# Optimization experiments

Hardware: AMD Instinct MI355X
Metric: run time of the kernel (lower is better)

Reference implementation:

```python
import jax, jax.numpy as jnp
import numpy as np

N_NODES = 100000
N_EDGES = 3200000
N_GRAPHS = 5000
N_LAYERS = 2
BN_EPS = 1e-5


def setup_inputs() -> dict:
    key = jax.random.key(0)
    ks = jax.random.split(key, 20)
    inp = {}
    inp['x'] = jax.random.normal(ks[0], (N_NODES, 14), dtype=jnp.float32)
    inp['edge_index'] = jax.random.randint(ks[1], (2, N_EDGES), 0, N_NODES, dtype=jnp.int64)
    inp['edge_attr'] = jax.random.uniform(ks[2], (N_EDGES, 3), dtype=jnp.float32)
    inp['batch'] = jnp.sort(jax.random.randint(ks[3], (N_NODES,), 0, N_GRAPHS, dtype=jnp.int64))
    s = 0.1
    inp['node_w'] = jax.random.normal(ks[4], (14, 32), dtype=jnp.float32) * s
    inp['node_b'] = jnp.zeros((32,), dtype=jnp.float32)
    inp['edge_w'] = jax.random.normal(ks[5], (3, 32), dtype=jnp.float32) * s
    inp['edge_b'] = jnp.zeros((32,), dtype=jnp.float32)
    inp['conv_w1'] = jax.random.normal(ks[6], (N_LAYERS, 32, 75), dtype=jnp.float32) * s
    inp['conv_b1'] = jnp.zeros((N_LAYERS, 75), dtype=jnp.float32)
    inp['conv_w2'] = jax.random.normal(ks[7], (N_LAYERS, 75, 32), dtype=jnp.float32) * s
    inp['conv_b2'] = jnp.zeros((N_LAYERS, 32), dtype=jnp.float32)
    inp['bn_g'] = jnp.ones((N_LAYERS, 32), dtype=jnp.float32)
    inp['bn_b'] = jnp.zeros((N_LAYERS, 32), dtype=jnp.float32)
    inp['lin1_w'] = jax.random.normal(ks[8], (32, 16), dtype=jnp.float32) * s
    inp['lin1_b'] = jnp.zeros((16,), dtype=jnp.float32)
    inp['lin2_w'] = jax.random.normal(ks[9], (16, 2), dtype=jnp.float32) * s
    inp['lin2_b'] = jnp.zeros((2,), dtype=jnp.float32)
    return inp


def _forward(x, edge_attr, node_w, node_b, edge_w, edge_b,
             conv_w1, conv_b1, conv_w2, conv_b2, bn_g, bn_b,
             lin1_w, lin1_b, lin2_w, lin2_b, edge_index, batch):
    src, dst = edge_index[0], edge_index[1]
    h = x @ node_w + node_b                      # [N, 32]
    ea = edge_attr @ edge_w + edge_b             # [E, 32]
    for l in range(N_LAYERS):
        # GINEConv (eps=0): nn(x_i + sum_j relu(x_j + e_ji))
        msg = jax.nn.relu(h[src] + ea)           # [E, 32]
        agg = jax.ops.segment_sum(msg, dst, num_segments=N_NODES)
        z = h + agg
        z = jax.nn.relu(z @ conv_w1[l] + conv_b1[l]) @ conv_w2[l] + conv_b2[l]
        # BatchNorm1d (training-mode batch statistics)
        mu = jnp.mean(z, axis=0)
        var = jnp.var(z, axis=0)
        z = (z - mu) * jax.lax.rsqrt(var + BN_EPS) * bn_g[l] + bn_b[l]
        h = jax.nn.relu(z)
    # global_mean_pool
    sums = jax.ops.segment_sum(h, batch, num_segments=N_GRAPHS)   # [G, 32]
    counts = jax.ops.segment_sum(jnp.ones((h.shape[0],), h.dtype), batch, num_segments=N_GRAPHS)
    graph_x = sums / jnp.maximum(counts, 1.0)[:, None]
    pred = jax.nn.relu(graph_x @ lin1_w + lin1_b) @ lin2_w + lin2_b  # [G, 2]
    return pred


def reference(x, edge_index, edge_attr, batch, node_w, node_b, edge_w, edge_b,
              conv_w1, conv_b1, conv_w2, conv_b2, bn_g, bn_b,
              lin1_w, lin1_b, lin2_w, lin2_b):
    return _forward(x, edge_attr, node_w, node_b, edge_w, edge_b,
                    conv_w1, conv_b1, conv_w2, conv_b2, bn_g, bn_b,
                    lin1_w, lin1_b, lin2_w, lin2_b, edge_index, batch)
```

## Files before the change

### kernel.cpp

```cpp
#include <hip/hip_runtime.h>
#include <hip/hip_fp16.h>

#define N_NODES 100000
#define N_EDGES 3200000
#define N_GRAPHS 5000
#define BN_EPS 1e-5f
#define HPAD 80
#define CHUNK 2048
#define NBLKA 1563
#define NBKT 392
#define NPAD2 (NBKT * 256)
#define NBLK_TOT (NBKT * NBLKA)
#define NS1 2394
#define LALLOC (NS1 * 256)
#define W1S 36

__global__ void k_encode(const float* __restrict__ x, const float* __restrict__ W,
                         const float* __restrict__ b, float* __restrict__ h,
                         __half* __restrict__ h16) {
    __shared__ float sW[448];
    __shared__ float sb[32];
    for (int i = threadIdx.x; i < 448; i += 256) sW[i] = W[i];
    if (threadIdx.x < 32) sb[threadIdx.x] = b[threadIdx.x];
    __syncthreads();
    int n = blockIdx.x * 256 + threadIdx.x;
    if (n >= N_NODES) return;
    float xi[14];
#pragma unroll
    for (int k = 0; k < 14; k++) xi[k] = x[n * 14 + k];
    float4* hp = (float4*)(h + (size_t)n * 32);
    __half2* hq = (__half2*)(h16 + (size_t)n * 32);
#pragma unroll
    for (int q = 0; q < 8; q++) {
        float4 acc;
        float* ap = (float*)&acc;
#pragma unroll
        for (int i = 0; i < 4; i++) {
            int c = q * 4 + i;
            float a = sb[c];
#pragma unroll
            for (int k = 0; k < 14; k++) a += xi[k] * sW[k * 32 + c];
            ap[i] = a;
        }
        hp[q] = acc;
        hq[q * 2 + 0] = __floats2half2_rn(acc.x, acc.y);
        hq[q * 2 + 1] = __floats2half2_rn(acc.z, acc.w);
    }
}

__global__ void k_prep(const float* __restrict__ W1, const float* __restrict__ b1,
                       const float* __restrict__ W2,
                       float* __restrict__ w1tp, float* __restrict__ b1p,
                       float* __restrict__ w2p) {
    int i = blockIdx.x * 256 + threadIdx.x;
    if (i < 2 * HPAD * 32) {
        int l = i / (HPAD * 32), r = i % (HPAD * 32);
        int j = r / 32, c = r % 32;
        w1tp[i] = (j < 75) ? W1[l * 2400 + c * 75 + j] : 0.f;
        w2p[i]  = (j < 75) ? W2[l * 2400 + j * 32 + c] : 0.f;
    } else if (i < 2 * HPAD * 32 + 2 * HPAD) {
        int k = i - 2 * HPAD * 32;
        int l = k / HPAD, j = k % HPAD;
        b1p[k] = (j < 75) ? b1[l * 75 + j] : 0.f;
    }
}

__global__ void __launch_bounds__(256) ksA(const int* __restrict__ ei, int* __restrict__ cmat) {
    __shared__ int lh[NBKT];
    for (int i = threadIdx.x; i < NBKT; i += 256) lh[i] = 0;
    __syncthreads();
    int b0 = blockIdx.x * CHUNK;
    for (int i = threadIdx.x; i < CHUNK; i += 256) {
        int e = b0 + i;
        if (e < N_EDGES) atomicAdd(&lh[ei[N_EDGES + e] >> 8], 1);
    }
    __syncthreads();
    for (int i = threadIdx.x; i < NBKT; i += 256)
        cmat[i * NBLKA + blockIdx.x] = lh[i];
}

__global__ void ks1(const int* __restrict__ a, int* __restrict__ bs) {
    __shared__ int s[256];
    int i = blockIdx.x * 256 + threadIdx.x;
    s[threadIdx.x] = a[i];
    __syncthreads();
    for (int o = 128; o > 0; o >>= 1) {
        if (threadIdx.x < o) s[threadIdx.x] += s[threadIdx.x + o];
        __syncthreads();
    }
    if (threadIdx.x == 0) bs[blockIdx.x] = s[0];
}

template<int NSX, int VPTX>
__global__ void ks2(int* __restrict__ bs) {
    __shared__ int s[256];
    int t = threadIdx.x;
    int v[VPTX];
    int base = t * VPTX, sum = 0;
#pragma unroll
    for (int k = 0; k < VPTX; k++) {
        int idx = base + k;
        int x = (idx < NSX) ? bs[idx] : 0;
        v[k] = sum; sum += x;
    }
    s[t] = sum;
    __syncthreads();
    for (int o = 1; o < 256; o <<= 1) {
        int add = (t >= o) ? s[t - o] : 0;
        __syncthreads();
        s[t] += add;
        __syncthreads();
    }
    int excl = (t == 0) ? 0 : s[t - 1];
#pragma unroll
    for (int k = 0; k < VPTX; k++) {
        int idx = base + k;
        if (idx < NSX) bs[idx] = excl + v[k];
    }
}

__global__ void ks3(int* __restrict__ a, const int* __restrict__ bs) {
    __shared__ int s[256];
    int t = threadIdx.x, i = blockIdx.x * 256 + t;
    int v = a[i];
    s[t] = v;
    __syncthreads();
    for (int o = 1; o < 256; o <<= 1) {
        int add = (t >= o) ? s[t - o] : 0;
        __syncthreads();
        s[t] += add;
        __syncthreads();
    }
    a[i] = s[t] - v + bs[blockIdx.x];
}

__global__ void __launch_bounds__(256) ksB(const int* __restrict__ ei, const float* __restrict__ ea,
                                           const int* __restrict__ cmat, float4* __restrict__ buf1,
                                           unsigned char* __restrict__ key) {
    __shared__ float4 rec[CHUNK];
    __shared__ unsigned short sbkt[CHUNK];
    __shared__ int lh[NBKT];
    __shared__ int lex[NBKT];
    __shared__ int gb[NBKT];
    __shared__ int sc[256];
    int t = threadIdx.x;
    int b0 = blockIdx.x * CHUNK;
    int nval = min(CHUNK, N_EDGES - b0);
    for (int i = t; i < NBKT; i += 256) lh[i] = 0;
    __syncthreads();
    for (int i = t; i < nval; i += 256)
        atomicAdd(&lh[ei[N_EDGES + b0 + i] >> 8], 1);
    __syncthreads();
    int x0 = (t * 2 < NBKT) ? lh[t * 2] : 0;
    int x1 = (t * 2 + 1 < NBKT) ? lh[t * 2 + 1] : 0;
    int v0 = 0, v1 = x0, run = x0 + x1;
    sc[t] = run;
    __syncthreads();
    for (int o = 1; o < 256; o <<= 1) {
        int add = (t >= o) ? sc[t - o] : 0;
        __syncthreads();
        sc[t] += add;
        __syncthreads();
    }
    int excl = (t == 0) ? 0 : sc[t - 1];
    if (t * 2 < NBKT) {
        int base = excl + v0;
        lex[t * 2] = base; lh[t * 2] = base;
        gb[t * 2] = cmat[(t * 2) * NBLKA + blockIdx.x];
    }
    if (t * 2 + 1 < NBKT) {
        int base = excl + v1;
        lex[t * 2 + 1] = base; lh[t * 2 + 1] = base;
        gb[t * 2 + 1] = cmat[(t * 2 + 1) * NBLKA + blockIdx.x];
    }
    __syncthreads();
    for (int i = t; i < nval; i += 256) {
        int e = b0 + i;
        int src = ei[e], dst = ei[N_EDGES + e];
        float a0 = ea[(size_t)e * 3 + 0], a1 = ea[(size_t)e * 3 + 1], a2 = ea[(size_t)e * 3 + 2];
        int bkt = dst >> 8;
        int r = atomicAdd(&lh[bkt], 1);
        rec[r] = make_float4(a0, a1, a2, __int_as_float(src | ((dst & 255) << 17)));
        sbkt[r] = (unsigned short)bkt;
    }
    __syncthreads();
    for (int p = t; p < nval; p += 256) {
        int bkt = sbkt[p];
        int gp = gb[bkt] + (p - lex[bkt]);
        float4 r = rec[p];
        buf1[gp] = r;
        key[gp] = (unsigned char)(((unsigned)__float_as_int(r.w)) >> 17);
    }
}

__global__ void __launch_bounds__(512) ksC(const int* __restrict__ cmat, const float4* __restrict__ buf1,
                                           const unsigned char* __restrict__ key,
                                           float4* __restrict__ packed, int* __restrict__ offs) {
    __shared__ int cnt[256];
    __shared__ int sc2[256];
    __shared__ int excl[256];
    int g = blockIdx.x, t = threadIdx.x;
    int bb = cmat[g * NBLKA];
    int be = (g == NBKT - 1) ? N_EDGES : cmat[(g + 1) * NBLKA];
    if (t < 256) cnt[t] = 0;
    __syncthreads();
    for (int j = bb + t; j < be; j += 512) atomicAdd(&cnt[key[j]], 1);
    __syncthreads();
    if (t < 256) sc2[t] = cnt[t];
    __syncthreads();
    for (int o = 1; o < 256; o <<= 1) {
        int add = 0;
        if (t < 256 && t >= o) add = sc2[t - o];
        __syncthreads();
        if (t < 256) sc2[t] += add;
        __syncthreads();
    }
    if (t < 256) {
        excl[t] = sc2[t] - cnt[t];
        offs[(g << 8) + t] = bb + excl[t];
        cnt[t] = 0;
    }
    if (g == NBKT - 1 && t == 0) offs[NPAD2] = N_EDGES;
    __syncthreads();
    for (int j = bb + t; j < be; j += 512) {
        float4 r = buf1[j];
        int bits = __float_as_int(r.w);
        int dl = bits >> 17;
        int rank = atomicAdd(&cnt[dl], 1);
        packed[bb + excl[dl] + rank] = make_float4(r.x, r.y, r.z, __int_as_float(bits & 0x1FFFF));
    }
}

template<bool BN>
__global__ void __launch_bounds__(256) k_agg(const float4* __restrict__ packed,
                                             const int* __restrict__ offs,
                                             const float* __restrict__ eW, const float* __restrict__ eb,
                                             const __half* __restrict__ h16,
                                             const float* __restrict__ hs,
                                             const float* __restrict__ stats,
                                             const float* __restrict__ bng, const float* __restrict__ bnb,
                                             float* __restrict__ zin) {
    int t = blockIdx.x * 256 + threadIdx.x;
    int n = t >> 5, s = t & 31;
    int q = s & 7, part = s >> 3;
    int c0 = q * 4;
    float w0[4], w1[4], w2[4], bb4[4];
#pragma unroll
    for (int i = 0; i < 4; i++) {
        w0[i] = eW[c0 + i];
        w1[i] = eW[32 + c0 + i];
        w2[i] = eW[64 + c0 + i];
        bb4[i] = eb[c0 + i];
    }
    int beg = offs[n], end = offs[n + 1];
    float acc0[4] = {0.f, 0.f, 0.f, 0.f};
    float acc1[4] = {0.f, 0.f, 0.f, 0.f};
    int j = beg + part;
    for (; j + 4 < end; j += 8) {
        float4 pa = packed[j];
        float4 pb = packed[j + 4];
        float2 ra = *(const float2*)(h16 + (size_t)__float_as_int(pa.w) * 32 + c0);
        float2 rb = *(const float2*)(h16 + (size_t)__float_as_int(pb.w) * 32 + c0);
        float2 a01 = __half22float2(*(__half2*)&ra.x);
        float2 a23 = __half22float2(*(__half2*)&ra.y);
        float2 b01 = __half22float2(*(__half2*)&rb.x);
        float2 b23 = __half22float2(*(__half2*)&rb.y);
        float ha4[4] = {a01.x, a01.y, a23.x, a23.y};
        float hb4[4] = {b01.x, b01.y, b23.x, b23.y};
#pragma unroll
        for (int i = 0; i < 4; i++) {
            acc0[i] += fmaxf(ha4[i] + pa.x * w0[i] + pa.y * w1[i] + pa.z * w2[i] + bb4[i], 0.f);
            acc1[i] += fmaxf(hb4[i] + pb.x * w0[i] + pb.y * w1[i] + pb.z * w2[i] + bb4[i], 0.f);
        }
    }
    if (j < end) {
        float4 p = packed[j];
        float2 r = *(const float2*)(h16 + (size_t)__float_as_int(p.w) * 32 + c0);
        float2 a01 = __half22float2(*(__half2*)&r.x);
        float2 a23 = __half22float2(*(__half2*)&r.y);
        float hp4[4] = {a01.x, a01.y, a23.x, a23.y};
#pragma unroll
        for (int i = 0; i < 4; i++)
            acc0[i] += fmaxf(hp4[i] + p.x * w0[i] + p.y * w1[i] + p.z * w2[i] + bb4[i], 0.f);
    }
    float acc[4];
#pragma unroll
    for (int i = 0; i < 4; i++) {
        acc[i] = acc0[i] + acc1[i];
        acc[i] += __shfl_xor(acc[i], 8, 64);
        acc[i] += __shfl_xor(acc[i], 16, 64);
    }
    if (part == 0) {
        float4 hq = *(const float4*)(hs + (size_t)n * 32 + c0);
        float* hp = (float*)&hq;
        float sv[4];
        if (BN) {
            const float invN = 1.0f / (float)N_NODES;
#pragma unroll
            for (int i = 0; i < 4; i++) {
                int c = c0 + i;
                float mu = stats[c] * invN;
                float var = stats[32 + c] * invN - mu * mu;
                float scl = bng[c] / sqrtf(var + BN_EPS);
                float sft = bnb[c] - mu * scl;
                sv[i] = fmaxf(hp[i] * scl + sft, 0.f);
            }
        } else {
#pragma unroll
            for (int i = 0; i < 4; i++) sv[i] = hp[i];
        }
        *(float4*)(zin + (size_t)n * 32 + c0) =
            make_float4(acc[0] + sv[0], acc[1] + sv[1], acc[2] + sv[2], acc[3] + sv[3]);
    }
}

__global__ void __launch_bounds__(256, 2) k_mlp(float* __restrict__ zio,
                                                const float* __restrict__ W1, const float* __restrict__ B1,
                                                const float* __restrict__ W2, const float* __restrict__ b2) {
    __shared__ float sW1[HPAD * W1S];
    __shared__ float sW2[2560];
    __shared__ float sB1[80];
    __shared__ float sb2[32];
    __shared__ float hidL[64 * 84];
    for (int i = threadIdx.x; i < 2560; i += 256) {
        int j = i >> 5, c = i & 31;
        sW1[j * W1S + c] = W1[i];
        sW2[i] = W2[i];
    }
    if (threadIdx.x < 80) sB1[threadIdx.x] = B1[threadIdx.x];
    if (threadIdx.x < 32) sb2[threadIdx.x] = b2[threadIdx.x];
    __syncthreads();
    unsigned lane = threadIdx.x & 63;
    unsigned wv = threadIdx.x >> 6;
    unsigned oct = lane >> 3;
    unsigned nd = lane & 7;
    unsigned nA = blockIdx.x * 64 + wv * 16 + nd;
    unsigned nB = nA + 8;
    bool vA = nA < N_NODES, vB = nB < N_NODES;
    unsigned nAc = vA ? nA : (N_NODES - 1);
    unsigned nBc = vB ? nB : (N_NODES - 1);
    const float4* apA = (const float4*)(zio + (size_t)nAc * 32);
    const float4* apB = (const float4*)(zio + (size_t)nBc * 32);
    float4 zA0 = apA[0], zA1 = apA[1], zA2 = apA[2], zA3 = apA[3];
    float4 zA4 = apA[4], zA5 = apA[5], zA6 = apA[6], zA7 = apA[7];
    float4 zB0 = apB[0], zB1 = apB[1], zB2 = apB[2], zB3 = apB[3];
    float4 zB4 = apB[4], zB5 = apB[5], zB6 = apB[6], zB7 = apB[7];
    float* hrowA = &hidL[(wv * 16 + nd) * 84];
    float* hrowB = &hidL[(wv * 16 + 8 + nd) * 84];
#pragma unroll
    for (int i = 0; i < 10; i++) {
        int j = (int)oct * 10 + i;
        const float4* wp = (const float4*)(sW1 + j * W1S);
        float a0 = 0.f, a1 = 0.f, a2 = 0.f, a3 = 0.f;
        float b0 = 0.f, b1v = 0.f, b2v = 0.f, b3 = 0.f;
#define MLP_STEP(Q, ZA, ZB)                                   \
        { float4 w4 = wp[Q];                                  \
          a0 += ZA.x * w4.x; a1 += ZA.y * w4.y;               \
          a2 += ZA.z * w4.z; a3 += ZA.w * w4.w;               \
          b0 += ZB.x * w4.x; b1v += ZB.y * w4.y;              \
          b2v += ZB.z * w4.z; b3 += ZB.w * w4.w; }
        MLP_STEP(0, zA0, zB0)
        MLP_STEP(1, zA1, zB1)
        MLP_STEP(2, zA2, zB2)
        MLP_STEP(3, zA3, zB3)
        MLP_STEP(4, zA4, zB4)
        MLP_STEP(5, zA5, zB5)
        MLP_STEP(6, zA6, zB6)
        MLP_STEP(7, zA7, zB7)
#undef MLP_STEP
        float bias = sB1[j];
        hrowA[oct * 10 + i] = fmaxf(bias + ((a0 + a1) + (a2 + a3)), 0.f);
        hrowB[oct * 10 + i] = fmaxf(bias + ((b0 + b1v) + (b2v + b3)), 0.f);
    }
    float4 zoA = *(const float4*)(sb2 + oct * 4);
    float4 zoB = zoA;
    const float4* hvA4 = (const float4*)hrowA;
    const float4* hvB4 = (const float4*)hrowB;
#pragma unroll
    for (int k = 0; k < 20; k++) {
        float4 ha = hvA4[k];
        float4 hb = hvB4[k];
        const float* wr = sW2 + (k * 4) * 32 + oct * 4;
        float4 wa = *(const float4*)(wr);
        float4 wb = *(const float4*)(wr + 32);
        float4 wc = *(const float4*)(wr + 64);
        float4 wd = *(const float4*)(wr + 96);
        zoA.x += ha.x * wa.x + ha.y * wb.x + ha.z * wc.x + ha.w * wd.x;
        zoA.y += ha.x * wa.y + ha.y * wb.y + ha.z * wc.y + ha.w * wd.y;
        zoA.z += ha.x * wa.z + ha.y * wb.z + ha.z * wc.z + ha.w * wd.z;
        zoA.w += ha.x * wa.w + ha.y * wb.w + ha.z * wc.w + ha.w * wd.w;
        zoB.x += hb.x * wa.x + hb.y * wb.x + hb.z * wc.x + hb.w * wd.x;
        zoB.y += hb.x * wa.y + hb.y * wb.y + hb.z * wc.y + hb.w * wd.y;
        zoB.z += hb.x * wa.z + hb.y * wb.z + hb.z * wc.z + hb.w * wd.z;
        zoB.w += hb.x * wa.w + hb.y * wb.w + hb.z * wc.w + hb.w * wd.w;
    }
    if (vA) *(float4*)(zio + (size_t)nA * 32 + oct * 4) = zoA;
    if (vB) *(float4*)(zio + (size_t)nB * 32 + oct * 4) = zoB;
}

__global__ void __launch_bounds__(256) k_stats(const float* __restrict__ z, float* __restrict__ stats) {
    __shared__ float ls[4 * 64];
    int tid = threadIdx.x;
    int c = tid & 31;
    float s = 0.f, s2 = 0.f;
    for (int e = blockIdx.x * 256 + tid; e < N_NODES * 32; e += 256 * 256) {
        float v = z[e];
        s += v; s2 += v * v;
    }
    s += __shfl_down(s, 32, 64);
    s2 += __shfl_down(s2, 32, 64);
    int wave = tid >> 6, lane = tid & 63;
    if (lane < 32) { ls[wave * 64 + c] = s; ls[wave * 64 + 32 + c] = s2; }
    __syncthreads();
    if (tid < 64) {
        float a = ls[tid] + ls[64 + tid] + ls[128 + tid] + ls[192 + tid];
        atomicAdd(&stats[tid], a);
    }
}

__global__ void k_bnh(const float* __restrict__ z, __half* __restrict__ m,
                      const float* __restrict__ stats, const float* __restrict__ g,
                      const float* __restrict__ b) {
    int t = blockIdx.x * 256 + threadIdx.x;
    if (t >= N_NODES * 8) return;
    int q = t & 7;
    float4 zv = ((const float4*)z)[t];
    float* zp = (float*)&zv;
    float ov[4];
    const float invN = 1.0f / (float)N_NODES;
#pragma unroll
    for (int i = 0; i < 4; i++) {
        int c = q * 4 + i;
        float mu = stats[c] * invN;
        float var = stats[32 + c] * invN - mu * mu;
        float sc = g[c] / sqrtf(var + BN_EPS);
        ov[i] = fmaxf((zp[i] - mu) * sc + b[c], 0.f);
    }
    __half2* hq = (__half2*)(m + (size_t)t * 4);
    hq[0] = __floats2half2_rn(ov[0], ov[1]);
    hq[1] = __floats2half2_rn(ov[2], ov[3]);
}

__global__ void k_goff(const int* __restrict__ batch, int* __restrict__ goff) {
    int g = blockIdx.x * 256 + threadIdx.x;
    if (g > N_GRAPHS) return;
    int lo = 0, hi = N_NODES;
    while (lo < hi) {
        int mid = (lo + hi) >> 1;
        if (batch[mid] < g) lo = mid + 1; else hi = mid;
    }
    goff[g] = lo;
}

__global__ void __launch_bounds__(256) k_pool2(const float* __restrict__ z, const int* __restrict__ goff,
                                               const float* __restrict__ stats,
                                               const float* __restrict__ g, const float* __restrict__ b,
                                               float* __restrict__ gsum) {
    int wid = threadIdx.x >> 6, lane = threadIdx.x & 63;
    int gi = blockIdx.x * 4 + wid;
    if (gi >= N_GRAPHS) return;
    int s = goff[gi], e = goff[gi + 1];
    int c = lane & 31, half = lane >> 5;
    const float invN = 1.0f / (float)N_NODES;
    float mu = stats[c] * invN;
    float var = stats[32 + c] * invN - mu * mu;
    float scl = g[c] / sqrtf(var + BN_EPS);
    float sft = b[c] - mu * scl;
    float acc = 0.f;
    for (int n = s + half; n < e; n += 2)
        acc += fmaxf(z[(size_t)n * 32 + c] * scl + sft, 0.f);
    acc += __shfl_down(acc, 32, 64);
    if (lane < 32) gsum[(size_t)gi * 32 + c] = acc;
}

__global__ void k_head(const float* __restrict__ gsum, const int* __restrict__ goff,
                       const float* __restrict__ W1, const float* __restrict__ b1,
                       const float* __restrict__ W2, const float* __restrict__ b2,
                       float* __restrict__ out) {
    __shared__ float sW1[512], sb1[16], sW2[32], sb2[2];
    for (int i = threadIdx.x; i < 512; i += 256) sW1[i] = W1[i];
    if (threadIdx.x < 16) sb1[threadIdx.x] = b1[threadIdx.x];
    if (threadIdx.x < 32) sW2[threadIdx.x] = W2[threadIdx.x];
    if (threadIdx.x < 2) sb2[threadIdx.x] = b2[threadIdx.x];
    __syncthreads();
    int gI = blockIdx.x * 256 + threadIdx.x;
    if (gI >= N_GRAPHS) return;
    float cnt = (float)(goff[gI + 1] - goff[gI]);
    float inv = 1.0f / fmaxf(cnt, 1.0f);
    float gx[32];
#pragma unroll
    for (int c = 0; c < 32; c++) gx[c] = gsum[(size_t)gI * 32 + c] * inv;
    float hid[16];
#pragma unroll
    for (int j = 0; j < 16; j++) {
        float a = sb1[j];
#pragma unroll
        for (int c = 0; c < 32; c++) a += gx[c] * sW1[c * 16 + j];
        hid[j] = fmaxf(a, 0.f);
    }
#pragma unroll
    for (int o = 0; o < 2; o++) {
        float a = sb2[o];
#pragma unroll
        for (int j = 0; j < 16; j++) a += hid[j] * sW2[j * 2 + o];
        out[(size_t)gI * 2 + o] = a;
    }
}

extern "C" void kernel_launch(void* const* d_in, const int* in_sizes, int n_in,
                              void* d_out, int out_size, void* d_ws, size_t ws_size,
                              hipStream_t stream) {
    const float* x       = (const float*)d_in[0];
    const int*   ei      = (const int*)d_in[1];
    const float* eattr   = (const float*)d_in[2];
    const int*   batch   = (const int*)d_in[3];
    const float* node_w  = (const float*)d_in[4];
    const float* node_b  = (const float*)d_in[5];
    const float* edge_w  = (const float*)d_in[6];
    const float* edge_b  = (const float*)d_in[7];
    const float* conv_w1 = (const float*)d_in[8];
    const float* conv_b1 = (const float*)d_in[9];
    const float* conv_w2 = (const float*)d_in[10];
    const float* conv_b2 = (const float*)d_in[11];
    const float* bn_g    = (const float*)d_in[12];
    const float* bn_b    = (const float*)d_in[13];
    const float* lin1_w  = (const float*)d_in[14];
    const float* lin1_b  = (const float*)d_in[15];
    const float* lin2_w  = (const float*)d_in[16];
    const float* lin2_b  = (const float*)d_in[17];
    float* out = (float*)d_out;

    float4* buf1    = (float4*)d_ws;
    float4* packed  = buf1 + N_EDGES;
    float*  h       = (float*)(packed + N_EDGES);
    float*  agg     = h + (size_t)N_NODES * 32;
    __half* m16     = (__half*)(agg + (size_t)N_NODES * 32);
    unsigned char* key = (unsigned char*)(m16 + (size_t)N_NODES * 32);
    int*    cmat    = (int*)(key + N_EDGES);
    float*  stats   = (float*)(cmat + LALLOC);
    int*    t1      = (int*)(stats + 128);
    int*    offs    = t1 + 2560;
    int*    goff    = offs + NPAD2 + 1;
    float*  gsum    = (float*)(goff + N_GRAPHS + 1);
    float*  w1tp    = gsum + (size_t)N_GRAPHS * 32;
    float*  b1p     = w1tp + 2 * HPAD * 32;
    float*  w2p     = b1p + 2 * HPAD;

    int nb_nodes = (N_NODES + 255) / 256;
    int nb_vec   = (N_NODES * 8 + 255) / 256;
    int nb_mlp   = (N_NODES + 63) / 64;

    hipMemsetAsync(cmat + NBLK_TOT, 0, (size_t)(LALLOC - NBLK_TOT + 128) * sizeof(int), stream);
    k_encode<<<nb_nodes, 256, 0, stream>>>(x, node_w, node_b, h, m16);
    k_prep<<<(2 * HPAD * 32 + 2 * HPAD + 255) / 256, 256, 0, stream>>>(
        conv_w1, conv_b1, conv_w2, w1tp, b1p, w2p);
    k_goff<<<(N_GRAPHS + 1 + 255) / 256, 256, 0, stream>>>(batch, goff);

    ksA<<<NBLKA, 256, 0, stream>>>(ei, cmat);
    ks1<<<NS1, 256, 0, stream>>>(cmat, t1);
    ks2<NS1, 10><<<1, 256, 0, stream>>>(t1);
    ks3<<<NS1, 256, 0, stream>>>(cmat, t1);
    ksB<<<NBLKA, 256, 0, stream>>>(ei, eattr, cmat, buf1, key);
    ksC<<<NBKT, 512, 0, stream>>>(cmat, buf1, key, packed, offs);

    k_agg<false><<<N_NODES * 32 / 256, 256, 0, stream>>>(packed, offs, edge_w, edge_b,
                                                         m16, h, stats, bn_g, bn_b, agg);
    k_mlp<<<nb_mlp, 256, 0, stream>>>(agg, w1tp, b1p, w2p, conv_b2);
    k_stats<<<256, 256, 0, stream>>>(agg, stats);
    k_bnh<<<nb_vec, 256, 0, stream>>>(agg, m16, stats, bn_g, bn_b);
    k_agg<true><<<N_NODES * 32 / 256, 256, 0, stream>>>(packed, offs, edge_w, edge_b,
                                                        m16, agg, stats, bn_g, bn_b, h);
    k_mlp<<<nb_mlp, 256, 0, stream>>>(h, w1tp + HPAD * 32, b1p + HPAD,
                                      w2p + HPAD * 32, conv_b2 + 32);
    k_stats<<<256, 256, 0, stream>>>(h, stats + 64);
    k_pool2<<<(N_GRAPHS + 3) / 4, 256, 0, stream>>>(h, goff, stats + 64, bn_g + 32, bn_b + 32, gsum);
    k_head<<<(N_GRAPHS + 255) / 256, 256, 0, stream>>>(gsum, goff, lin1_w, lin1_b, lin2_w, lin2_b, out);
}
```

Baseline: 477.8 us.

## Fuse setup kernels, fold BN stats into MLP, merge pool and head

Merges the encode, weight-prep and graph-offset kernels into one launch. The MLP kernel now emits per-block partial sums and squares, and a small reduction kernel replaces the full re-read of z done by the old stats pass. Pooling and the prediction head are combined into one kernel. The gather index math is also narrowed to 32-bit. These changes cut launch count and one full pass over node features, at the cost of an extra partial-stats buffer and a different summation order.

```diff
diff --git a/kernel.cpp b/kernel.cpp
--- a/kernel.cpp
+++ b/kernel.cpp
@@ -14,54 +14,70 @@
 #define NS1 2394
 #define LALLOC (NS1 * 256)
 #define W1S 36
-
-__global__ void k_encode(const float* __restrict__ x, const float* __restrict__ W,
-                         const float* __restrict__ b, float* __restrict__ h,
-                         __half* __restrict__ h16) {
-    __shared__ float sW[448];
-    __shared__ float sb[32];
-    for (int i = threadIdx.x; i < 448; i += 256) sW[i] = W[i];
-    if (threadIdx.x < 32) sb[threadIdx.x] = b[threadIdx.x];
-    __syncthreads();
-    int n = blockIdx.x * 256 + threadIdx.x;
-    if (n >= N_NODES) return;
-    float xi[14];
-#pragma unroll
-    for (int k = 0; k < 14; k++) xi[k] = x[n * 14 + k];
-    float4* hp = (float4*)(h + (size_t)n * 32);
-    __half2* hq = (__half2*)(h16 + (size_t)n * 32);
-#pragma unroll
-    for (int q = 0; q < 8; q++) {
-        float4 acc;
-        float* ap = (float*)&acc;
-#pragma unroll
-        for (int i = 0; i < 4; i++) {
-            int c = q * 4 + i;
-            float a = sb[c];
-#pragma unroll
-            for (int k = 0; k < 14; k++) a += xi[k] * sW[k * 32 + c];
-            ap[i] = a;
+#define NB_ENC 391
+#define NBMLP 1563
+#define PSROW 1568
+
+__global__ void __launch_bounds__(256) k_setup(const float* __restrict__ x, const float* __restrict__ nW,
+                                               const float* __restrict__ nb, float* __restrict__ h,
+                                               __half* __restrict__ h16,
+                                               const float* __restrict__ W1, const float* __restrict__ b1,
+                                               const float* __restrict__ W2,
+                                               float* __restrict__ w1tp, float* __restrict__ b1p,
+                                               float* __restrict__ w2p,
+                                               const int* __restrict__ batch, int* __restrict__ goff) {
+    int bid = blockIdx.x;
+    if (bid < NB_ENC) {
+        __shared__ float sW[448];
+        __shared__ float sb[32];
+        for (int i = threadIdx.x; i < 448; i += 256) sW[i] = nW[i];
+        if (threadIdx.x < 32) sb[threadIdx.x] = nb[threadIdx.x];
+        __syncthreads();
+        int n = bid * 256 + threadIdx.x;
+        if (n >= N_NODES) return;
+        float xi[14];
+#pragma unroll
+        for (int k = 0; k < 14; k++) xi[k] = x[n * 14 + k];
+        float4* hp = (float4*)(h + (size_t)n * 32);
+        __half2* hq = (__half2*)(h16 + (size_t)n * 32);
+#pragma unroll
+        for (int q = 0; q < 8; q++) {
+            float4 acc;
+            float* ap = (float*)&acc;
+#pragma unroll
+            for (int i = 0; i < 4; i++) {
+                int c = q * 4 + i;
+                float a = sb[c];
+#pragma unroll
+                for (int k = 0; k < 14; k++) a += xi[k] * sW[k * 32 + c];
+                ap[i] = a;
+            }
+            hp[q] = acc;
+            hq[q * 2 + 0] = __floats2half2_rn(acc.x, acc.y);
+            hq[q * 2 + 1] = __floats2half2_rn(acc.z, acc.w);
         }
-        hp[q] = acc;
-        hq[q * 2 + 0] = __floats2half2_rn(acc.x, acc.y);
-        hq[q * 2 + 1] = __floats2half2_rn(acc.z, acc.w);
-    }
-}
-
-__global__ void k_prep(const float* __restrict__ W1, const float* __restrict__ b1,
-                       const float* __restrict__ W2,
-                       float* __restrict__ w1tp, float* __restrict__ b1p,
-                       float* __restrict__ w2p) {
-    int i = blockIdx.x * 256 + threadIdx.x;
-    if (i < 2 * HPAD * 32) {
-        int l = i / (HPAD * 32), r = i % (HPAD * 32);
-        int j = r / 32, c = r % 32;
-        w1tp[i] = (j < 75) ? W1[l * 2400 + c * 75 + j] : 0.f;
-        w2p[i]  = (j < 75) ? W2[l * 2400 + j * 32 + c] : 0.f;
-    } else if (i < 2 * HPAD * 32 + 2 * HPAD) {
-        int k = i - 2 * HPAD * 32;
-        int l = k / HPAD, j = k % HPAD;
-        b1p[k] = (j < 75) ? b1[l * 75 + j] : 0.f;
+    } else if (bid == NB_ENC) {
+        for (int i = threadIdx.x; i < 2 * HPAD * 32 + 2 * HPAD; i += 256) {
+            if (i < 2 * HPAD * 32) {
+                int l = i / (HPAD * 32), r = i % (HPAD * 32);
+                int j = r / 32, c = r % 32;
+                w1tp[i] = (j < 75) ? W1[l * 2400 + c * 75 + j] : 0.f;
+                w2p[i]  = (j < 75) ? W2[l * 2400 + j * 32 + c] : 0.f;
+            } else {
+                int k = i - 2 * HPAD * 32;
+                int l = k / HPAD, j = k % HPAD;
+                b1p[k] = (j < 75) ? b1[l * 75 + j] : 0.f;
+            }
+        }
+    } else {
+        for (int g = threadIdx.x; g <= N_GRAPHS; g += 256) {
+            int lo = 0, hi = N_NODES;
+            while (lo < hi) {
+                int mid = (lo + hi) >> 1;
+                if (batch[mid] < g) lo = mid + 1; else hi = mid;
+            }
+            goff[g] = lo;
+        }
     }
 }
 
@@ -259,8 +275,10 @@
     for (; j + 4 < end; j += 8) {
         float4 pa = packed[j];
         float4 pb = packed[j + 4];
-        float2 ra = *(const float2*)(h16 + (size_t)__float_as_int(pa.w) * 32 + c0);
-        float2 rb = *(const float2*)(h16 + (size_t)__float_as_int(pb.w) * 32 + c0);
+        unsigned offa = ((unsigned)__float_as_int(pa.w) << 5) + (unsigned)c0;
+        unsigned offb = ((unsigned)__float_as_int(pb.w) << 5) + (unsigned)c0;
+        float2 ra = *(const float2*)(h16 + offa);
+        float2 rb = *(const float2*)(h16 + offb);
         float2 a01 = __half22float2(*(__half2*)&ra.x);
         float2 a23 = __half22float2(*(__half2*)&ra.y);
         float2 b01 = __half22float2(*(__half2*)&rb.x);
@@ -275,7 +293,8 @@
     }
     if (j < end) {
         float4 p = packed[j];
-        float2 r = *(const float2*)(h16 + (size_t)__float_as_int(p.w) * 32 + c0);
+        unsigned offp = ((unsigned)__float_as_int(p.w) << 5) + (unsigned)c0;
+        float2 r = *(const float2*)(h16 + offp);
         float2 a01 = __half22float2(*(__half2*)&r.x);
         float2 a23 = __half22float2(*(__half2*)&r.y);
         float hp4[4] = {a01.x, a01.y, a23.x, a23.y};
@@ -316,12 +335,15 @@
 
 __global__ void __launch_bounds__(256, 2) k_mlp(float* __restrict__ zio,
                                                 const float* __restrict__ W1, const float* __restrict__ B1,
-                                                const float* __restrict__ W2, const float* __restrict__ b2) {
+                                                const float* __restrict__ W2, const float* __restrict__ b2,
+                                                float* __restrict__ pstat) {
     __shared__ float sW1[HPAD * W1S];
     __shared__ float sW2[2560];
     __shared__ float sB1[80];
     __shared__ float sb2[32];
     __shared__ float hidL[64 * 84];
+    __shared__ float psum[4][32];
+    __shared__ float psq[4][32];
     for (int i = threadIdx.x; i < 2560; i += 256) {
         int j = i >> 5, c = i & 31;
         sW1[j * W1S + c] = W1[i];
@@ -396,26 +418,50 @@
     }
     if (vA) *(float4*)(zio + (size_t)nA * 32 + oct * 4) = zoA;
     if (vB) *(float4*)(zio + (size_t)nB * 32 + oct * 4) = zoB;
-}
-
-__global__ void __launch_bounds__(256) k_stats(const float* __restrict__ z, float* __restrict__ stats) {
-    __shared__ float ls[4 * 64];
-    int tid = threadIdx.x;
-    int c = tid & 31;
-    float s = 0.f, s2 = 0.f;
-    for (int e = blockIdx.x * 256 + tid; e < N_NODES * 32; e += 256 * 256) {
-        float v = z[e];
-        s += v; s2 += v * v;
-    }
-    s += __shfl_down(s, 32, 64);
-    s2 += __shfl_down(s2, 32, 64);
-    int wave = tid >> 6, lane = tid & 63;
-    if (lane < 32) { ls[wave * 64 + c] = s; ls[wave * 64 + 32 + c] = s2; }
-    __syncthreads();
-    if (tid < 64) {
-        float a = ls[tid] + ls[64 + tid] + ls[128 + tid] + ls[192 + tid];
-        atomicAdd(&stats[tid], a);
-    }
+    float s0 = (vA ? zoA.x : 0.f) + (vB ? zoB.x : 0.f);
+    float s1 = (vA ? zoA.y : 0.f) + (vB ? zoB.y : 0.f);
+    float s2 = (vA ? zoA.z : 0.f) + (vB ? zoB.z : 0.f);
+    float s3 = (vA ? zoA.w : 0.f) + (vB ? zoB.w : 0.f);
+    float q0 = (vA ? zoA.x * zoA.x : 0.f) + (vB ? zoB.x * zoB.x : 0.f);
+    float q1 = (vA ? zoA.y * zoA.y : 0.f) + (vB ? zoB.y * zoB.y : 0.f);
+    float q2 = (vA ? zoA.z * zoA.z : 0.f) + (vB ? zoB.z * zoB.z : 0.f);
+    float q3 = (vA ? zoA.w * zoA.w : 0.f) + (vB ? zoB.w * zoB.w : 0.f);
+#pragma unroll
+    for (int m = 1; m < 8; m <<= 1) {
+        s0 += __shfl_xor(s0, m, 64); s1 += __shfl_xor(s1, m, 64);
+        s2 += __shfl_xor(s2, m, 64); s3 += __shfl_xor(s3, m, 64);
+        q0 += __shfl_xor(q0, m, 64); q1 += __shfl_xor(q1, m, 64);
+        q2 += __shfl_xor(q2, m, 64); q3 += __shfl_xor(q3, m, 64);
+    }
+    if (nd == 0) {
+        psum[wv][oct * 4 + 0] = s0; psum[wv][oct * 4 + 1] = s1;
+        psum[wv][oct * 4 + 2] = s2; psum[wv][oct * 4 + 3] = s3;
+        psq[wv][oct * 4 + 0] = q0;  psq[wv][oct * 4 + 1] = q1;
+        psq[wv][oct * 4 + 2] = q2;  psq[wv][oct * 4 + 3] = q3;
+    }
+    __syncthreads();
+    if (threadIdx.x < 32) {
+        int c = threadIdx.x;
+        pstat[(size_t)c * PSROW + blockIdx.x] =
+            psum[0][c] + psum[1][c] + psum[2][c] + psum[3][c];
+    } else if (threadIdx.x < 64) {
+        int c = threadIdx.x - 32;
+        pstat[(size_t)(32 + c) * PSROW + blockIdx.x] =
+            psq[0][c] + psq[1][c] + psq[2][c] + psq[3][c];
+    }
+}
+
+__global__ void __launch_bounds__(256) k_statsR(const float* __restrict__ pstat, float* __restrict__ stats) {
+    __shared__ float ls[4];
+    int r = blockIdx.x;
+    const float* row = pstat + (size_t)r * PSROW;
+    float s = 0.f;
+    for (int i = threadIdx.x; i < NBMLP; i += 256) s += row[i];
+#pragma unroll
+    for (int m = 1; m < 64; m <<= 1) s += __shfl_xor(s, m, 64);
+    if ((threadIdx.x & 63) == 0) ls[threadIdx.x >> 6] = s;
+    __syncthreads();
+    if (threadIdx.x == 0) stats[r] = ls[0] + ls[1] + ls[2] + ls[3];
 }
 
 __global__ void k_bnh(const float* __restrict__ z, __half* __restrict__ m,
@@ -441,69 +487,52 @@
     hq[1] = __floats2half2_rn(ov[2], ov[3]);
 }
 
-__global__ void k_goff(const int* __restrict__ batch, int* __restrict__ goff) {
-    int g = blockIdx.x * 256 + threadIdx.x;
-    if (g > N_GRAPHS) return;
-    int lo = 0, hi = N_NODES;
-    while (lo < hi) {
-        int mid = (lo + hi) >> 1;
-        if (batch[mid] < g) lo = mid + 1; else hi = mid;
-    }
-    goff[g] = lo;
-}
-
-__global__ void __launch_bounds__(256) k_pool2(const float* __restrict__ z, const int* __restrict__ goff,
-                                               const float* __restrict__ stats,
-                                               const float* __restrict__ g, const float* __restrict__ b,
-                                               float* __restrict__ gsum) {
+__global__ void __launch_bounds__(256) k_poolhead(const float* __restrict__ z, const int* __restrict__ goff,
+                                                  const float* __restrict__ stats,
+                                                  const float* __restrict__ bg, const float* __restrict__ bb,
+                                                  const float* __restrict__ W1, const float* __restrict__ b1,
+                                                  const float* __restrict__ W2, const float* __restrict__ b2,
+                                                  float* __restrict__ out) {
+    __shared__ float sW1[512];
+    __shared__ float sb1[16], sW2[32], sb2[2];
+    __shared__ float gxs[4][32];
+    for (int i = threadIdx.x; i < 512; i += 256) sW1[i] = W1[i];
+    if (threadIdx.x < 16) sb1[threadIdx.x] = b1[threadIdx.x];
+    if (threadIdx.x < 32) sW2[threadIdx.x] = W2[threadIdx.x];
+    if (threadIdx.x < 2) sb2[threadIdx.x] = b2[threadIdx.x];
+    __syncthreads();
     int wid = threadIdx.x >> 6, lane = threadIdx.x & 63;
     int gi = blockIdx.x * 4 + wid;
-    if (gi >= N_GRAPHS) return;
     int s = goff[gi], e = goff[gi + 1];
     int c = lane & 31, half = lane >> 5;
     const float invN = 1.0f / (float)N_NODES;
     float mu = stats[c] * invN;
     float var = stats[32 + c] * invN - mu * mu;
-    float scl = g[c] / sqrtf(var + BN_EPS);
-    float sft = b[c] - mu * scl;
+    float scl = bg[c] / sqrtf(var + BN_EPS);
+    float sft = bb[c] - mu * scl;
     float acc = 0.f;
     for (int n = s + half; n < e; n += 2)
         acc += fmaxf(z[(size_t)n * 32 + c] * scl + sft, 0.f);
     acc += __shfl_down(acc, 32, 64);
-    if (lane < 32) gsum[(size_t)gi * 32 + c] = acc;
-}
-
-__global__ void k_head(const float* __restrict__ gsum, const int* __restrict__ goff,
-                       const float* __restrict__ W1, const float* __restrict__ b1,
-                       const float* __restrict__ W2, const float* __restrict__ b2,
-                       float* __restrict__ out) {
-    __shared__ float sW1[512], sb1[16], sW2[32], sb2[2];
-    for (int i = threadIdx.x; i < 512; i += 256) sW1[i] = W1[i];
-    if (threadIdx.x < 16) sb1[threadIdx.x] = b1[threadIdx.x];
-    if (threadIdx.x < 32) sW2[threadIdx.x] = W2[threadIdx.x];
-    if (threadIdx.x < 2) sb2[threadIdx.x] = b2[threadIdx.x];
-    __syncthreads();
-    int gI = blockIdx.x * 256 + threadIdx.x;
-    if (gI >= N_GRAPHS) return;
-    float cnt = (float)(goff[gI + 1] - goff[gI]);
-    float inv = 1.0f / fmaxf(cnt, 1.0f);
-    float gx[32];
-#pragma unroll
-    for (int c = 0; c < 32; c++) gx[c] = gsum[(size_t)gI * 32 + c] * inv;
-    float hid[16];
-#pragma unroll
-    for (int j = 0; j < 16; j++) {
-        float a = sb1[j];
-#pragma unroll
-        for (int c = 0; c < 32; c++) a += gx[c] * sW1[c * 16 + j];
-        hid[j] = fmaxf(a, 0.f);
-    }
-#pragma unroll
-    for (int o = 0; o < 2; o++) {
-        float a = sb2[o];
-#pragma unroll
-        for (int j = 0; j < 16; j++) a += hid[j] * sW2[j * 2 + o];
-        out[(size_t)gI * 2 + o] = a;
+    float inv = 1.0f / fmaxf((float)(e - s), 1.0f);
+    if (lane < 32) gxs[wid][c] = acc * inv;
+    float hid = 0.f;
+    if (lane < 16) {
+        float a = sb1[lane];
+#pragma unroll
+        for (int cc = 0; cc < 32; cc++) a += gxs[wid][cc] * sW1[cc * 16 + lane];
+        hid = fmaxf(a, 0.f);
+    }
+    float p0 = 0.f, p1 = 0.f;
+    if (lane < 16) { p0 = hid * sW2[lane * 2 + 0]; p1 = hid * sW2[lane * 2 + 1]; }
+#pragma unroll
+    for (int m = 1; m < 16; m <<= 1) {
+        p0 += __shfl_xor(p0, m, 64);
+        p1 += __shfl_xor(p1, m, 64);
+    }
+    if (lane == 0) {
+        out[(size_t)gi * 2 + 0] = p0 + sb2[0];
+        out[(size_t)gi * 2 + 1] = p1 + sb2[1];
     }
 }
 
@@ -541,20 +570,17 @@
     int*    t1      = (int*)(stats + 128);
     int*    offs    = t1 + 2560;
     int*    goff    = offs + NPAD2 + 1;
-    float*  gsum    = (float*)(goff + N_GRAPHS + 1);
-    float*  w1tp    = gsum + (size_t)N_GRAPHS * 32;
+    float*  pstat   = (float*)(goff + N_GRAPHS + 1);
+    float*  w1tp    = pstat + 64 * PSROW;
     float*  b1p     = w1tp + 2 * HPAD * 32;
     float*  w2p     = b1p + 2 * HPAD;
 
-    int nb_nodes = (N_NODES + 255) / 256;
-    int nb_vec   = (N_NODES * 8 + 255) / 256;
-    int nb_mlp   = (N_NODES + 63) / 64;
+    int nb_vec = (N_NODES * 8 + 255) / 256;
 
     hipMemsetAsync(cmat + NBLK_TOT, 0, (size_t)(LALLOC - NBLK_TOT + 128) * sizeof(int), stream);
-    k_encode<<<nb_nodes, 256, 0, stream>>>(x, node_w, node_b, h, m16);
-    k_prep<<<(2 * HPAD * 32 + 2 * HPAD + 255) / 256, 256, 0, stream>>>(
-        conv_w1, conv_b1, conv_w2, w1tp, b1p, w2p);
-    k_goff<<<(N_GRAPHS + 1 + 255) / 256, 256, 0, stream>>>(batch, goff);
+    k_setup<<<NB_ENC + 2, 256, 0, stream>>>(x, node_w, node_b, h, m16,
+                                            conv_w1, conv_b1, conv_w2, w1tp, b1p, w2p,
+                                            batch, goff);
 
     ksA<<<NBLKA, 256, 0, stream>>>(ei, cmat);
     ks1<<<NS1, 256, 0, stream>>>(cmat, t1);
@@ -565,14 +591,14 @@
 
     k_agg<false><<<N_NODES * 32 / 256, 256, 0, stream>>>(packed, offs, edge_w, edge_b,
                                                          m16, h, stats, bn_g, bn_b, agg);
-    k_mlp<<<nb_mlp, 256, 0, stream>>>(agg, w1tp, b1p, w2p, conv_b2);
-    k_stats<<<256, 256, 0, stream>>>(agg, stats);
+    k_mlp<<<NBMLP, 256, 0, stream>>>(agg, w1tp, b1p, w2p, conv_b2, pstat);
+    k_statsR<<<64, 256, 0, stream>>>(pstat, stats);
     k_bnh<<<nb_vec, 256, 0, stream>>>(agg, m16, stats, bn_g, bn_b);
     k_agg<true><<<N_NODES * 32 / 256, 256, 0, stream>>>(packed, offs, edge_w, edge_b,
                                                         m16, agg, stats, bn_g, bn_b, h);
-    k_mlp<<<nb_mlp, 256, 0, stream>>>(h, w1tp + HPAD * 32, b1p + HPAD,
-                                      w2p + HPAD * 32, conv_b2 + 32);
-    k_stats<<<256, 256, 0, stream>>>(h, stats + 64);
-    k_pool2<<<(N_GRAPHS + 3) / 4, 256, 0, stream>>>(h, goff, stats + 64, bn_g + 32, bn_b + 32, gsum);
-    k_head<<<(N_GRAPHS + 255) / 256, 256, 0, stream>>>(gsum, goff, lin1_w, lin1_b, lin2_w, lin2_b, out);
-}
+    k_mlp<<<NBMLP, 256, 0, stream>>>(h, w1tp + HPAD * 32, b1p + HPAD,
+                                     w2p + HPAD * 32, conv_b2 + 32, pstat);
+    k_statsR<<<64, 256, 0, stream>>>(pstat, stats + 64);
+    k_poolhead<<<N_GRAPHS / 4, 256, 0, stream>>>(h, goff, stats + 64, bn_g + 32, bn_b + 32,
+                                                 lin1_w, lin1_b, lin2_w, lin2_b, out);
+}
```

Result: slower. 540.1 us (+13.0%).
